# Kernel optimization log

Hardware: AMD Instinct MI355X
Metric: run time of the kernel (lower is better)

The kernel has to match this reference:

```python
import jax, jax.numpy as jnp
import numpy as np
import math

N = 20000          # real nodes (batch_size)
D = 256            # hidden_dim
H = 4              # num_heads
L = 3              # num_layers
E = 320000         # local edges
EXP_DEG = 4        # expander_degree
LN_EPS = 1e-5


def setup_inputs() -> dict:
    key = jax.random.key(0)
    ks = jax.random.split(key, 8)
    x = jax.random.normal(ks[0], (N, D), jnp.float32)
    rng = np.random.default_rng(0)
    edge_index = jnp.asarray(rng.integers(0, N, size=(2, E)), dtype=jnp.int32)
    # Expander: EXP_DEG//2 random permutations on N+1 nodes (incl. virtual node),
    # each contributing edges in both directions -> degree-EXP_DEG regular graph.
    n = N + 1
    perms = [rng.permutation(n) for _ in range(EXP_DEG // 2)]
    src = np.concatenate([np.arange(n) for _ in perms] + perms)
    dst = np.concatenate(perms + [np.arange(n) for _ in perms])
    exp_edge_index = jnp.asarray(np.stack([src, dst]), dtype=jnp.int32)
    s_in = 1.0 / math.sqrt(D)
    s_ffn = 1.0 / math.sqrt(4 * D)
    def w(k, shape, s):
        return jax.random.normal(k, shape, jnp.float32) * s
    params = {
        'Wqkv_loc': w(ks[1], (L, D, 3 * D), s_in), 'bqkv_loc': jnp.zeros((L, 3 * D), jnp.float32),
        'Wo_loc':   w(ks[2], (L, D, D), s_in),     'bo_loc':   jnp.zeros((L, D), jnp.float32),
        'Wqkv_exp': w(ks[3], (L, D, 3 * D), s_in), 'bqkv_exp': jnp.zeros((L, 3 * D), jnp.float32),
        'Wo_exp':   w(ks[4], (L, D, D), s_in),     'bo_exp':   jnp.zeros((L, D), jnp.float32),
        'ln_g': jnp.ones((L, D), jnp.float32),     'ln_b': jnp.zeros((L, D), jnp.float32),
        'W1': w(ks[5], (L, D, 4 * D), s_in),       'b1': jnp.zeros((L, 4 * D), jnp.float32),
        'W2': w(ks[6], (L, 4 * D, D), s_ffn),      'b2': jnp.zeros((L, D), jnp.float32),
    }
    return {'x': x, 'edge_index': edge_index, 'exp_edge_index': exp_edge_index, **params}


def _attention(h, src, dst, Wqkv, bqkv, Wo, bo):
    # Sparse multi-head attention over (src -> dst) edges with segment softmax per dst.
    n, d = h.shape
    dh = d // H
    qkv = (h @ Wqkv + bqkv).reshape(n, 3, H, dh)
    q, k, v = qkv[:, 0], qkv[:, 1], qkv[:, 2]            # [n, H, dh]
    score = (q[dst] * k[src]).sum(-1) / jnp.sqrt(jnp.float32(dh))  # [e, H]
    m = jax.ops.segment_max(score, dst, num_segments=n)  # [n, H]
    ex = jnp.exp(score - m[dst])
    denom = jax.ops.segment_sum(ex, dst, num_segments=n)
    alpha = ex / (denom[dst] + 1e-16)
    out = jax.ops.segment_sum(alpha[:, :, None] * v[src], dst, num_segments=n)  # [n, H, dh]
    return out.reshape(n, d) @ Wo + bo


def _layer_norm(x, g, b):
    mu = x.mean(-1, keepdims=True)
    var = ((x - mu) ** 2).mean(-1, keepdims=True)
    return (x - mu) * jax.lax.rsqrt(var + LN_EPS) * g + b


def reference(x, edge_index, exp_edge_index, Wqkv_loc, bqkv_loc, Wo_loc, bo_loc,
              Wqkv_exp, bqkv_exp, Wo_exp, bo_exp, ln_g, ln_b, W1, b1, W2, b2):
    n0 = x.shape[0]
    # VirtualNode transform: append one zero-feature node connected to/from all nodes.
    h = jnp.concatenate([x, jnp.zeros((1, x.shape[1]), x.dtype)], axis=0)
    ar = jnp.arange(n0, dtype=edge_index.dtype)
    vn = jnp.full((n0,), n0, dtype=edge_index.dtype)
    src = jnp.concatenate([edge_index[0], ar, vn])
    dst = jnp.concatenate([edge_index[1], vn, ar])
    esrc, edst = exp_edge_index[0], exp_edge_index[1]
    for l in range(L):  # fixed small number of structurally distinct layers
        res = h
        loc = _attention(h, src, dst, Wqkv_loc[l], bqkv_loc[l], Wo_loc[l], bo_loc[l])
        exp = _attention(h, esrc, edst, Wqkv_exp[l], bqkv_exp[l], Wo_exp[l], bo_exp[l])
        h = _layer_norm(res + loc + exp, ln_g[l], ln_b[l])
        h = h + (jax.nn.gelu(h @ W1[l] + b1[l], approximate=False) @ W2[l] + b2[l])
    return h[:n0]
```

## Files before the change

### kernel.cpp

```cpp
#include <hip/hip_runtime.h>
#include <stdint.h>

#define NREAL   20000
#define NNODES  20001
#define VN      20000
#define E_EDGES 320000
#define NEXP    80004
#define MPAD    20096
#define NVNW    320

typedef unsigned short u16;
typedef unsigned int   u32;
typedef __bf16 bf16x8 __attribute__((ext_vector_type(8)));
typedef float  f32x4  __attribute__((ext_vector_type(4)));
typedef u16    u16x8  __attribute__((ext_vector_type(8)));

__device__ __host__ __forceinline__ size_t fmoff(int row, int col, int LD) {
    return (size_t)(row >> 4) * ((size_t)LD * 16) + (size_t)((col >> 3) * 128)
         + (size_t)((row & 15) * 8) + (size_t)(col & 7);
}

__device__ __forceinline__ int qkv_perm(int n) {
    if (n < 256) return n;
    int u = n - 256;
    int part = u >> 8;
    int cl = u & 255;
    return 256 + (cl >> 2) * 8 + part * 4 + (cl & 3);
}

__device__ __forceinline__ float bf2f(u16 v) {
    union { u32 u; float f; } x; x.u = ((u32)v) << 16; return x.f;
}
__device__ __forceinline__ u16 f2bf(float f) {
    union { float f; u32 u; } x; x.f = f;
    u32 r = (x.u + 0x7fffu + ((x.u >> 16) & 1u)) >> 16;
    return (u16)r;
}
__device__ __forceinline__ float4 cvt4(ushort4 u) {
    return make_float4(bf2f(u.x), bf2f(u.y), bf2f(u.z), bf2f(u.w));
}
__device__ __forceinline__ float4 ld4bf(const u16* p) { return cvt4(*(const ushort4*)p); }
__device__ __forceinline__ float4 cvtk8(u16x8 r) {
    return make_float4(bf2f(r[0]), bf2f(r[1]), bf2f(r[2]), bf2f(r[3]));
}
__device__ __forceinline__ float4 cvtv8(u16x8 r) {
    return make_float4(bf2f(r[4]), bf2f(r[5]), bf2f(r[6]), bf2f(r[7]));
}


__global__ void hinit_kernel(const float* __restrict__ x, float* __restrict__ h,
                             u16* __restrict__ hb) {
    int idx = blockIdx.x * 256 + threadIdx.x;
    if (idx >= NNODES * 64) return;
    int row = idx >> 6, c0 = (idx & 63) * 4;
    float4 v = make_float4(0.f, 0.f, 0.f, 0.f);
    if (row < NREAL) v = *(const float4*)(x + (size_t)row * 256 + c0);
    *(float4*)(h + (size_t)row * 256 + c0) = v;
    ushort4 o;
    o.x = f2bf(v.x); o.y = f2bf(v.y); o.z = f2bf(v.z); o.w = f2bf(v.w);
    *(ushort4*)(hb + fmoff(row, c0, 256)) = o;
}

__global__ void init_kernel(int* cnt, int* fill, int* ecnt,
                            const float* __restrict__ bl, const float* __restrict__ be,
                            float* __restrict__ bcat,
                            const float* __restrict__ bol, const float* __restrict__ boe,
                            float* __restrict__ bsum) {
    int i = blockIdx.x * 256 + threadIdx.x;
    if (i < NREAL) { cnt[i] = 0; fill[i] = 0; }
    if (i < NNODES) ecnt[i] = 0;
    if (i < 3 * 1536) {
        int l = i / 1536, c = i - l * 1536;
        float v = (c < 768) ? bl[l * 768 + c] : be[l * 768 + c - 768];
        int cc = (c >= 768) ? c - 768 : c;
        int d = qkv_perm(cc) + ((c >= 768) ? 768 : 0);
        bcat[l * 1536 + d] = v;
    }
    if (i < 3 * 256) bsum[i] = bol[i] + boe[i];
}

__global__ void csr_count_kernel(const int* __restrict__ ei, int* __restrict__ cnt) {
    int e = blockIdx.x * 256 + threadIdx.x;
    if (e < E_EDGES) atomicAdd(&cnt[ei[E_EDGES + e]], 1);
}

__global__ void csr_scan_kernel(const int* __restrict__ cnt, int* __restrict__ indptr) {
    __shared__ int ssum[256];
    int t = threadIdx.x;
    int c0 = t * 79;
    int s = 0;
    for (int j = 0; j < 79; j++) {
        int i = c0 + j;
        if (i < NREAL) s += cnt[i];
    }
    ssum[t] = s;
    __syncthreads();
    for (int d2 = 1; d2 < 256; d2 <<= 1) {
        int v = (t >= d2) ? ssum[t - d2] : 0;
        __syncthreads();
        ssum[t] += v;
        __syncthreads();
    }
    int run = (t == 0) ? 0 : ssum[t - 1];
    for (int j = 0; j < 79; j++) {
        int i = c0 + j;
        if (i < NREAL) { indptr[i] = run; run += cnt[i]; }
    }
    if (t == 255) indptr[NREAL] = run;
}

__global__ void csr_scatter_kernel(const int* __restrict__ ei, const int* __restrict__ indptr,
                                   int* __restrict__ fill, int* __restrict__ srcs) {
    int e = blockIdx.x * 256 + threadIdx.x;
    if (e < E_EDGES) {
        int d = ei[E_EDGES + e];
        int pos = indptr[d] + atomicAdd(&fill[d], 1);
        srcs[pos] = ei[e];
    }
}

__global__ void exp_scatter_kernel(const int* __restrict__ eei, int* __restrict__ ecnt,
                                   int* __restrict__ esrcs) {
    int e = blockIdx.x * 256 + threadIdx.x;
    if (e < NEXP) {
        int d = eei[NEXP + e];
        int pos = atomicAdd(&ecnt[d], 1);
        esrcs[d * 4 + pos] = eei[e];
    }
}

__global__ void wconv_all_kernel(const float* __restrict__ WqkvL, const float* __restrict__ WqkvE,
                                 const float* __restrict__ WoL, const float* __restrict__ WoE,
                                 const float* __restrict__ W1, const float* __restrict__ W2,
                                 u16* __restrict__ out) {
    int i = blockIdx.x * 256 + threadIdx.x;
    if (i >= 3 * 1048576) return;
    int l = i / 1048576, r = i - l * 1048576;
    if (r >= 393216 && r < 524288) {
        int r2 = r - 393216;
        int k = r2 >> 8, n = r2 & 255;
        float v = (k < 256) ? WoL[(size_t)l * 65536 + k * 256 + n]
                            : WoE[(size_t)l * 65536 + (k - 256) * 256 + n];
        out[(size_t)l * 1048576 + 393216 + fmoff(n, k, 512)] = f2bf(v);
        return;
    }
    const float* src; int K, N; int base;
    if (r < 196608)      { src = WqkvL; K = 256;  N = 768;  base = 0; }
    else if (r < 393216) { src = WqkvE; K = 256;  N = 768;  base = 196608; }
    else if (r < 786432) { src = W1;    K = 256;  N = 1024; base = 524288; }
    else                 { src = W2;    K = 1024; N = 256;  base = 786432; }
    int r2 = r - base;
    int k = r2 / N, n = r2 - k * N;
    int d = (r < 393216) ? qkv_perm(n) : n;
    out[(size_t)l * 1048576 + base + fmoff(d, k, K)] = f2bf(src[(size_t)l * K * N + r2]);
}

__global__ __launch_bounds__(256) void qkv_rw(
    const u16* __restrict__ A, const u16* __restrict__ Bt, const float* __restrict__ bias,
    u16* __restrict__ Q0, u16* __restrict__ KV0,
    u16* __restrict__ Q1, u16* __restrict__ KV1, int M) {
    const int lin = blockIdx.x;
    const int mt = lin / 6, ns = lin - mt * 6;
    const int tm = mt * 64;
    if (tm >= M) return;
    const int tid = threadIdx.x;
    const int w = tid >> 6, lane = tid & 63;
    const int lm = lane & 15, q = lane >> 4;

    f32x4 acc[4][4];
#pragma unroll
    for (int a = 0; a < 4; a++)
#pragma unroll
        for (int b = 0; b < 4; b++) acc[a][b] = (f32x4)0.0f;

    const u16* apf[4];
    const u16* bpf[4];
#pragma unroll
    for (int mi = 0; mi < 4; mi++)
        apf[mi] = A + (size_t)(tm / 16 + mi) * 4096 + q * 128 + lm * 8;
#pragma unroll
    for (int ni = 0; ni < 4; ni++)
        bpf[ni] = Bt + (size_t)(ns * 16 + w * 4 + ni) * 4096 + q * 128 + lm * 8;

    bf16x8 sA[3][4], sB[3][4];
#pragma unroll
    for (int s = 0; s < 2; s++) {
#pragma unroll
        for (int mi = 0; mi < 4; mi++) sA[s][mi] = *(const bf16x8*)(apf[mi] + s * 512);
#pragma unroll
        for (int ni = 0; ni < 4; ni++) sB[s][ni] = *(const bf16x8*)(bpf[ni] + s * 512);
    }
#pragma unroll
    for (int i = 0; i < 8; i++) {
        const int cu = i % 3, pf = (i + 2) % 3;
        if (i + 2 < 8) {
#pragma unroll
            for (int mi = 0; mi < 4; mi++) sA[pf][mi] = *(const bf16x8*)(apf[mi] + (i + 2) * 512);
#pragma unroll
            for (int ni = 0; ni < 4; ni++) sB[pf][ni] = *(const bf16x8*)(bpf[ni] + (i + 2) * 512);
        }
#pragma unroll
        for (int mi = 0; mi < 4; mi++)
#pragma unroll
            for (int ni = 0; ni < 4; ni++)
                acc[mi][ni] = __builtin_amdgcn_mfma_f32_16x16x32_bf16(
                    sB[cu][ni], sA[cu][mi], acc[mi][ni], 0, 0, 0);
    }

    float4 b4[4];
#pragma unroll
    for (int ni = 0; ni < 4; ni++)
        b4[ni] = *(const float4*)(bias + ns * 256 + w * 64 + ni * 16 + q * 4);

#pragma unroll
    for (int mi = 0; mi < 4; mi++) {
        int grow = tm + mi * 16 + lm;
        if (grow >= M) continue;
#pragma unroll
        for (int ni = 0; ni < 4; ni++) {
            int gcol = ns * 256 + w * 64 + ni * 16 + q * 4;
            float v0 = acc[mi][ni][0] + b4[ni].x;
            float v1 = acc[mi][ni][1] + b4[ni].y;
            float v2 = acc[mi][ni][2] + b4[ni].z;
            float v3 = acc[mi][ni][3] + b4[ni].w;
            ushort4 o;
            o.x = f2bf(v0); o.y = f2bf(v1); o.z = f2bf(v2); o.w = f2bf(v3);
            u16* dst;
            if (gcol < 256)       dst = Q0  + (size_t)grow * 256 + gcol;
            else if (gcol < 768)  dst = KV0 + (size_t)grow * 512 + (gcol - 256);
            else if (gcol < 1024) dst = Q1  + (size_t)grow * 256 + (gcol - 768);
            else                  dst = KV1 + (size_t)grow * 512 + (gcol - 1024);
            *(ushort4*)dst = o;
        }
    }
}

__global__ __launch_bounds__(256) void ffn1_rw(
    const u16* __restrict__ A, const u16* __restrict__ Bt, const float* __restrict__ bias,
    u16* __restrict__ Cb, int M) {
    const int lin = blockIdx.x;
    const int mt = lin >> 2, ns = lin & 3;
    const int tm = mt * 64;
    if (tm >= M) return;
    const int tid = threadIdx.x;
    const int w = tid >> 6, lane = tid & 63;
    const int lm = lane & 15, q = lane >> 4;

    f32x4 acc[4][4];
#pragma unroll
    for (int a = 0; a < 4; a++)
#pragma unroll
        for (int b = 0; b < 4; b++) acc[a][b] = (f32x4)0.0f;

    const u16* apf[4];
    const u16* bpf[4];
#pragma unroll
    for (int mi = 0; mi < 4; mi++)
        apf[mi] = A + (size_t)(tm / 16 + mi) * 4096 + q * 128 + lm * 8;
#pragma unroll
    for (int ni = 0; ni < 4; ni++)
        bpf[ni] = Bt + (size_t)(ns * 16 + w * 4 + ni) * 4096 + q * 128 + lm * 8;

    bf16x8 sA[3][4], sB[3][4];
#pragma unroll
    for (int s = 0; s < 2; s++) {
#pragma unroll
        for (int mi = 0; mi < 4; mi++) sA[s][mi] = *(const bf16x8*)(apf[mi] + s * 512);
#pragma unroll
        for (int ni = 0; ni < 4; ni++) sB[s][ni] = *(const bf16x8*)(bpf[ni] + s * 512);
    }
#pragma unroll
    for (int i = 0; i < 8; i++) {
        const int cu = i % 3, pf = (i + 2) % 3;
        if (i + 2 < 8) {
#pragma unroll
            for (int mi = 0; mi < 4; mi++) sA[pf][mi] = *(const bf16x8*)(apf[mi] + (i + 2) * 512);
#pragma unroll
            for (int ni = 0; ni < 4; ni++) sB[pf][ni] = *(const bf16x8*)(bpf[ni] + (i + 2) * 512);
        }
#pragma unroll
        for (int mi = 0; mi < 4; mi++)
#pragma unroll
            for (int ni = 0; ni < 4; ni++)
                acc[mi][ni] = __builtin_amdgcn_mfma_f32_16x16x32_bf16(
                    sB[cu][ni], sA[cu][mi], acc[mi][ni], 0, 0, 0);
    }

    float4 b4[4];
#pragma unroll
    for (int ni = 0; ni < 4; ni++)
        b4[ni] = *(const float4*)(bias + ns * 256 + w * 64 + ni * 16 + q * 4);

#pragma unroll
    for (int mi = 0; mi < 4; mi++) {
        int grow = tm + mi * 16 + lm;
        if (grow >= M) continue;
#pragma unroll
        for (int ni = 0; ni < 4; ni++) {
            int gcol = ns * 256 + w * 64 + ni * 16 + q * 4;
            float v0 = acc[mi][ni][0] + b4[ni].x;
            float v1 = acc[mi][ni][1] + b4[ni].y;
            float v2 = acc[mi][ni][2] + b4[ni].z;
            float v3 = acc[mi][ni][3] + b4[ni].w;
            float g0, g1, g2, g3;
            {
                float u = 0.7978845608f * (v0 + 0.044715f * v0 * v0 * v0);
                g0 = 0.5f * v0 * (2.0f - 2.0f / (__expf(2.0f * u) + 1.0f));
            }
            {
                float u = 0.7978845608f * (v1 + 0.044715f * v1 * v1 * v1);
                g1 = 0.5f * v1 * (2.0f - 2.0f / (__expf(2.0f * u) + 1.0f));
            }
            {
                float u = 0.7978845608f * (v2 + 0.044715f * v2 * v2 * v2);
                g2 = 0.5f * v2 * (2.0f - 2.0f / (__expf(2.0f * u) + 1.0f));
            }
            {
                float u = 0.7978845608f * (v3 + 0.044715f * v3 * v3 * v3);
                g3 = 0.5f * v3 * (2.0f - 2.0f / (__expf(2.0f * u) + 1.0f));
            }
            ushort4 o;
            o.x = f2bf(g0); o.y = f2bf(g1); o.z = f2bf(g2); o.w = f2bf(g3);
            *(ushort4*)(Cb + fmoff(grow, gcol, 1024)) = o;
        }
    }
}

template <int EPI, int K, int MT>
__global__ __launch_bounds__(256) void gemm_fm(
    const u16* __restrict__ A, const u16* __restrict__ Bt, const float* __restrict__ bias,
    u16* Cb, float* Cf, const float* resid, int M, int Nout, int nby) {
    constexpr int MFR = MT / 32;
    constexpr int NK = K / 32;
    const int lin = blockIdx.x;
    const int xcd = lin & 7, sub = lin >> 3;
    const int mtile = xcd + 8 * (sub / nby);
    const int ntile = sub - (sub / nby) * nby;
    const int tm = mtile * MT, tn = ntile * 128;
    if (tm >= M) return;

    const int tid = threadIdx.x;
    const int w = tid >> 6, lane = tid & 63;
    const int lm = lane & 15, q = lane >> 4;
    const int mo = (w >> 1) * (MT / 2), no = (w & 1) * 64;

    f32x4 acc[MFR][4];
#pragma unroll
    for (int a = 0; a < MFR; a++)
#pragma unroll
        for (int b = 0; b < 4; b++) acc[a][b] = (f32x4)0.0f;

    const u16* apf[MFR];
    const u16* bpf[4];
#pragma unroll
    for (int t = 0; t < MFR; t++) {
        int p = (tm + mo) / 16 + t;
        apf[t] = A + (size_t)p * (16 * K) + q * 128 + lm * 8;
    }
#pragma unroll
    for (int n = 0; n < 4; n++) {
        int c = (tn + no) / 16 + n;
        bpf[n] = Bt + (size_t)c * (16 * K) + q * 128 + lm * 8;
    }

    bf16x8 sA[3][MFR], sB[3][4];
#pragma unroll
    for (int s = 0; s < 2 && s < NK; s++) {
#pragma unroll
        for (int t = 0; t < MFR; t++) sA[s][t] = *(const bf16x8*)(apf[t] + s * 512);
#pragma unroll
        for (int n = 0; n < 4; n++) sB[s][n] = *(const bf16x8*)(bpf[n] + s * 512);
    }
#pragma unroll
    for (int i = 0; i < NK; i++) {
        const int cu = i % 3, pf = (i + 2) % 3;
        if (i + 2 < NK) {
#pragma unroll
            for (int t = 0; t < MFR; t++) sA[pf][t] = *(const bf16x8*)(apf[t] + (i + 2) * 512);
#pragma unroll
            for (int n = 0; n < 4; n++) sB[pf][n] = *(const bf16x8*)(bpf[n] + (i + 2) * 512);
        }
#pragma unroll
        for (int mi = 0; mi < MFR; mi++)
#pragma unroll
            for (int ni = 0; ni < 4; ni++)
                acc[mi][ni] = __builtin_amdgcn_mfma_f32_16x16x32_bf16(
                    sB[cu][ni], sA[cu][mi], acc[mi][ni], 0, 0, 0);
    }

    float4 b4[4];
#pragma unroll
    for (int ni = 0; ni < 4; ni++)
        b4[ni] = *(const float4*)(bias + tn + no + ni * 16 + q * 4);

#pragma unroll
    for (int mi = 0; mi < MFR; mi++) {
        int grow = tm + mo + mi * 16 + lm;
        if constexpr (EPI == 4) { if (grow >= NREAL) continue; }
        else                    { if (grow >= M) continue; }
#pragma unroll
        for (int ni = 0; ni < 4; ni++) {
            int gcol = tn + no + ni * 16 + q * 4;
            float v0 = acc[mi][ni][0] + b4[ni].x;
            float v1 = acc[mi][ni][1] + b4[ni].y;
            float v2 = acc[mi][ni][2] + b4[ni].z;
            float v3 = acc[mi][ni][3] + b4[ni].w;
            size_t idx = (size_t)grow * Nout + gcol;
            if constexpr (EPI == 1) {
                *(float4*)(Cf + idx) = make_float4(v0, v1, v2, v3);
            } else if constexpr (EPI == 3) {
                float4 rv = *(const float4*)(resid + idx);
                float o0 = rv.x + v0, o1 = rv.y + v1, o2 = rv.z + v2, o3 = rv.w + v3;
                *(float4*)(Cf + idx) = make_float4(o0, o1, o2, o3);
                ushort4 o;
                o.x = f2bf(o0); o.y = f2bf(o1); o.z = f2bf(o2); o.w = f2bf(o3);
                *(ushort4*)(Cb + fmoff(grow, gcol, Nout)) = o;
            } else {
                float4 rv = *(const float4*)(resid + idx);
                *(float4*)(Cf + idx) = make_float4(rv.x + v0, rv.y + v1, rv.z + v2, rv.w + v3);
            }
        }
    }
}

__global__ void vn_merge_kernel(const float* __restrict__ part, u16* __restrict__ acat) {
    __shared__ float sm[4][64][6];
    int w = threadIdx.x >> 6, lane = threadIdx.x & 63;
    int h = lane >> 4;
    int off = (h << 6) + (lane & 15) * 4;
    float M = -1e30f, L = 0.0f;
    float ax = 0, ay = 0, az = 0, aw = 0;
    for (int p = w * 80; p < w * 80 + 80; p++) {
        const float* pp = part + (size_t)p * 264;
        float pm = pp[h], pl = pp[4 + h];
        float4 nm = *(const float4*)(pp + 8 + off);
        float Mn = fmaxf(M, pm);
        float s0 = __expf(M - Mn);
        float s1 = __expf(pm - Mn);
        ax = ax * s0 + nm.x * s1;
        ay = ay * s0 + nm.y * s1;
        az = az * s0 + nm.z * s1;
        aw = aw * s0 + nm.w * s1;
        L = L * s0 + pl * s1;
        M = Mn;
    }
    sm[w][lane][0] = M; sm[w][lane][1] = L;
    sm[w][lane][2] = ax; sm[w][lane][3] = ay;
    sm[w][lane][4] = az; sm[w][lane][5] = aw;
    __syncthreads();
    if (w == 0) {
        float M2 = -1e30f, L2 = 0.0f;
        float bx = 0, by = 0, bz = 0, bw = 0;
#pragma unroll
        for (int p = 0; p < 4; p++) {
            float pm = sm[p][lane][0], pl = sm[p][lane][1];
            float Mn = fmaxf(M2, pm);
            float s0 = __expf(M2 - Mn);
            float s1 = __expf(pm - Mn);
            bx = bx * s0 + sm[p][lane][2] * s1;
            by = by * s0 + sm[p][lane][3] * s1;
            bz = bz * s0 + sm[p][lane][4] * s1;
            bw = bw * s0 + sm[p][lane][5] * s1;
            L2 = L2 * s0 + pl * s1;
            M2 = Mn;
        }
        float inv = 1.0f / (L2 + 1e-16f);
        ushort4 o;
        o.x = f2bf(bx * inv); o.y = f2bf(by * inv);
        o.z = f2bf(bz * inv); o.w = f2bf(bw * inv);
        *(ushort4*)(acat + fmoff(VN, off, 512)) = o;
    }
}

__global__ void attn_fused_kernel(const u16* __restrict__ qb_loc, const u16* __restrict__ kv_loc,
                                  const u16* __restrict__ qb_exp, const u16* __restrict__ kv_exp,
                                  const int* __restrict__ indptr, const int* __restrict__ srcs,
                                  const int* __restrict__ esrcs,
                                  u16* __restrict__ acat, float* __restrict__ part) {
    int gw0 = (int)((blockIdx.x * (size_t)blockDim.x + threadIdx.x) >> 6);
    int gw = __builtin_amdgcn_readfirstlane(gw0);
    int lane = threadIdx.x & 63;
    int h = lane >> 4;
    int off = (h << 6) + (lane & 15) * 4;
    int coff = (off >> 2) * 8;

    if (gw < NVNW) {
        int wv = gw;
        float4 qv = ld4bf(qb_loc + (size_t)VN * 256 + off);
        float m = -1e30f, l = 0.0f;
        float ax = 0, ay = 0, az = 0, aw = 0;
        for (int i = wv; i < NREAL; i += NVNW) {
            u16x8 r = *(const u16x8*)(kv_loc + (size_t)i * 512 + coff);
            float4 k4 = cvtk8(r);
            float4 v4 = cvtv8(r);
            float s = qv.x * k4.x + qv.y * k4.y + qv.z * k4.z + qv.w * k4.w;
            s += __shfl_xor(s, 1); s += __shfl_xor(s, 2);
            s += __shfl_xor(s, 4); s += __shfl_xor(s, 8);
            float sc = s * 0.125f;
            float mn = fmaxf(m, sc);
            float fold = __expf(m - mn);
            float ee = __expf(sc - mn);
            ax = ax * fold + v4.x * ee;
            ay = ay * fold + v4.y * ee;
            az = az * fold + v4.z * ee;
            aw = aw * fold + v4.w * ee;
            l = l * fold + ee;
            m = mn;
        }
        float* pp = part + (size_t)wv * 264;
        if ((lane & 15) == 0) { pp[h] = m; pp[4 + h] = l; }
        *(float4*)(pp + 8 + off) = make_float4(ax, ay, az, aw);
        return;
    }
    gw -= NVNW;

    const u16 *qb, *kv;
    const int* sl;
    int node, beg, deg, tot, cbase;
    if (gw < NREAL) {
        node = gw; qb = qb_loc; kv = kv_loc; sl = srcs; cbase = 0;
        beg = indptr[node]; deg = indptr[node + 1] - beg; tot = deg + 1;
    } else if (gw < NREAL + NNODES) {
        node = gw - NREAL;
        qb = qb_exp; kv = kv_exp; sl = esrcs; cbase = 256;
        beg = node * 4; deg = 4; tot = 4;
    } else {
        return;
    }

    float4 qv = ld4bf(qb + (size_t)node * 256 + off);
    float m = -1e30f, l = 0.0f;
    float ax = 0, ay = 0, az = 0, aw = 0;

    if (tot <= 4) {
        u16x8 raw[4];
#pragma unroll
        for (int j = 0; j < 4; j++) {
            int s = (j < deg) ? sl[beg + j] : VN;
            raw[j] = *(const u16x8*)(kv + (size_t)s * 512 + coff);
        }
        float sc[4];
#pragma unroll
        for (int j = 0; j < 4; j++) {
            float4 k4 = cvtk8(raw[j]);
            float p = qv.x * k4.x + qv.y * k4.y + qv.z * k4.z + qv.w * k4.w;
            p += __shfl_xor(p, 1); p += __shfl_xor(p, 2);
            p += __shfl_xor(p, 4); p += __shfl_xor(p, 8);
            sc[j] = (j < tot) ? p * 0.125f : -1e30f;
        }
        float mn = fmaxf(fmaxf(sc[0], sc[1]), fmaxf(sc[2], sc[3]));
#pragma unroll
        for (int j = 0; j < 4; j++) {
            float ee = __expf(sc[j] - mn);
            float4 v4 = cvtv8(raw[j]);
            ax += v4.x * ee; ay += v4.y * ee; az += v4.z * ee; aw += v4.w * ee;
            l += ee;
        }
        m = mn;
    } else {
        const int nch = (tot + 7) >> 3;
        u16x8 rA[8], rB[8];
#pragma unroll
        for (int j = 0; j < 8; j++) {
            int s = (j < deg) ? sl[beg + j] : VN;
            rA[j] = *(const u16x8*)(kv + (size_t)s * 512 + coff);
        }
        for (int c = 0; c < nch; c++) {
            if (c + 1 < nch) {
                const int e0n = (c + 1) * 8;
#pragma unroll
                for (int j = 0; j < 8; j++) {
                    int e = e0n + j;
                    int s = (e < deg) ? sl[beg + e] : VN;
                    rB[j] = *(const u16x8*)(kv + (size_t)s * 512 + coff);
                }
            }
            const int e0 = c * 8;
            float sc[8];
#pragma unroll
            for (int j = 0; j < 8; j++) {
                float4 k4 = cvtk8(rA[j]);
                float p = qv.x * k4.x + qv.y * k4.y + qv.z * k4.z + qv.w * k4.w;
                p += __shfl_xor(p, 1); p += __shfl_xor(p, 2);
                p += __shfl_xor(p, 4); p += __shfl_xor(p, 8);
                sc[j] = (e0 + j < tot) ? p * 0.125f : -1e30f;
            }
            float cmax = fmaxf(fmaxf(fmaxf(sc[0], sc[1]), fmaxf(sc[2], sc[3])),
                               fmaxf(fmaxf(sc[4], sc[5]), fmaxf(sc[6], sc[7])));
            float mn = fmaxf(m, cmax);
            float fold = __expf(m - mn);
            ax *= fold; ay *= fold; az *= fold; aw *= fold; l *= fold;
#pragma unroll
            for (int j = 0; j < 8; j++) {
                float ee = __expf(sc[j] - mn);
                float4 v4 = cvtv8(rA[j]);
                ax += v4.x * ee; ay += v4.y * ee; az += v4.z * ee; aw += v4.w * ee;
                l += ee;
            }
            m = mn;
#pragma unroll
            for (int j = 0; j < 8; j++) rA[j] = rB[j];
        }
    }
    float inv = 1.0f / (l + 1e-16f);
    ushort4 o;
    o.x = f2bf(ax * inv); o.y = f2bf(ay * inv);
    o.z = f2bf(az * inv); o.w = f2bf(aw * inv);
    *(ushort4*)(acat + fmoff(node, cbase + off, 512)) = o;
}

__global__ void ln_kernel(const float* hin, const float* __restrict__ asum,
                          const float* __restrict__ g, const float* __restrict__ b,
                          float* hout, u16* __restrict__ hb) {
    int row = blockIdx.x * 4 + (threadIdx.x >> 6);
    if (row >= NNODES) return;
    int lane = threadIdx.x & 63;
    size_t base = (size_t)row * 256 + lane * 4;
    float4 xv = *(const float4*)(hin + base);
    float4 av = *(const float4*)(asum + base);
    xv.x += av.x; xv.y += av.y; xv.z += av.z; xv.w += av.w;
    float s = xv.x + xv.y + xv.z + xv.w;
#pragma unroll
    for (int o = 1; o < 64; o <<= 1) s += __shfl_xor(s, o);
    float mu = s * (1.0f / 256.0f);
    float dx = xv.x - mu, dy = xv.y - mu, dz = xv.z - mu, dw = xv.w - mu;
    float ss = dx * dx + dy * dy + dz * dz + dw * dw;
#pragma unroll
    for (int o = 1; o < 64; o <<= 1) ss += __shfl_xor(ss, o);
    float var = ss * (1.0f / 256.0f);
    float inv = 1.0f / sqrtf(var + 1e-5f);
    float4 gv = *(const float4*)(g + lane * 4);
    float4 bv = *(const float4*)(b + lane * 4);
    float4 y;
    y.x = dx * inv * gv.x + bv.x;
    y.y = dy * inv * gv.y + bv.y;
    y.z = dz * inv * gv.z + bv.z;
    y.w = dw * inv * gv.w + bv.w;
    *(float4*)(hout + base) = y;
    ushort4 o4;
    o4.x = f2bf(y.x); o4.y = f2bf(y.y); o4.z = f2bf(y.z); o4.w = f2bf(y.w);
    *(ushort4*)(hb + fmoff(row, lane * 4, 256)) = o4;
}


extern "C" void kernel_launch(void* const* d_in, const int* in_sizes, int n_in,
                              void* d_out, int out_size, void* d_ws, size_t ws_size,
                              hipStream_t stream) {
    (void)in_sizes; (void)n_in; (void)out_size;
    const float* x        = (const float*)d_in[0];
    const int*   ei       = (const int*)d_in[1];
    const int*   eei      = (const int*)d_in[2];
    const float* Wqkv_loc = (const float*)d_in[3];
    const float* bqkv_loc = (const float*)d_in[4];
    const float* Wo_loc   = (const float*)d_in[5];
    const float* bo_loc   = (const float*)d_in[6];
    const float* Wqkv_exp = (const float*)d_in[7];
    const float* bqkv_exp = (const float*)d_in[8];
    const float* Wo_exp   = (const float*)d_in[9];
    const float* bo_exp   = (const float*)d_in[10];
    const float* ln_g     = (const float*)d_in[11];
    const float* ln_b     = (const float*)d_in[12];
    const float* W1       = (const float*)d_in[13];
    const float* b1       = (const float*)d_in[14];
    const float* W2       = (const float*)d_in[15];
    const float* b2       = (const float*)d_in[16];

    char* wsp = (char*)d_ws;
    size_t off = 0;
    auto carve = [&](size_t bytes) -> void* {
        void* p = wsp + off;
        off += (bytes + 255) & ~(size_t)255;
        return p;
    };
    float* h_f    = (float*)carve((size_t)NNODES * 256 * 4);
    u16*   h_b    = (u16*)carve((size_t)MPAD * 256 * 2);
    u16*   qb_loc = (u16*)carve((size_t)NNODES * 256 * 2);
    u16*   kv_loc = (u16*)carve((size_t)NNODES * 512 * 2);
    u16*   qb_exp = (u16*)carve((size_t)NNODES * 256 * 2);
    u16*   kv_exp = (u16*)carve((size_t)NNODES * 512 * 2);
    u16*   acat   = (u16*)carve((size_t)MPAD * 512 * 2);
    float* asum   = (float*)carve((size_t)NNODES * 256 * 4);
    u16*   wbf    = (u16*)carve((size_t)3 * 1048576 * 2);
    float* bcat   = (float*)carve((size_t)3 * 1536 * 4);
    float* bsum   = (float*)carve((size_t)3 * 256 * 4);
    int*   cnt    = (int*)carve((size_t)NREAL * 4);
    int*   indptr = (int*)carve((size_t)(NREAL + 1) * 4);
    int*   fill   = (int*)carve((size_t)NREAL * 4);
    int*   srcs   = (int*)carve((size_t)E_EDGES * 4);
    int*   ecnt   = (int*)carve((size_t)NNODES * 4);
    int*   esrcs  = (int*)carve((size_t)NNODES * 4 * 4);
    float* part   = (float*)carve((size_t)NVNW * 264 * 4);
    u16*   mid_d  = (u16*)carve((size_t)MPAD * 1024 * 2);
    u16*   mid    = (ws_size >= off) ? mid_d : qb_loc;

    hinit_kernel<<<(NNODES * 64 + 255) / 256, 256, 0, stream>>>(x, h_f, h_b);
    init_kernel<<<(NNODES + 255) / 256, 256, 0, stream>>>(
        cnt, fill, ecnt, bqkv_loc, bqkv_exp, bcat, bo_loc, bo_exp, bsum);
    csr_count_kernel<<<(E_EDGES + 255) / 256, 256, 0, stream>>>(ei, cnt);
    csr_scan_kernel<<<1, 256, 0, stream>>>(cnt, indptr);
    csr_scatter_kernel<<<(E_EDGES + 255) / 256, 256, 0, stream>>>(ei, indptr, fill, srcs);
    exp_scatter_kernel<<<(NEXP + 255) / 256, 256, 0, stream>>>(eei, ecnt, esrcs);
    wconv_all_kernel<<<(3 * 1048576 + 255) / 256, 256, 0, stream>>>(
        Wqkv_loc, Wqkv_exp, Wo_loc, Wo_exp, W1, W2, wbf);

    const int NBM64 = 320;
    const int ATTN_BLOCKS = (NVNW + NREAL + NNODES + 3) / 4;
    const int QKV_BLOCKS = (MPAD / 64) * 6;

    for (int l = 0; l < 3; l++) {
        const u16* wqkvC = wbf + (size_t)l * 1048576 + 0;
        const u16* wocat = wbf + (size_t)l * 1048576 + 393216;
        const u16* w1T   = wbf + (size_t)l * 1048576 + 524288;
        const u16* w2T   = wbf + (size_t)l * 1048576 + 786432;

        qkv_rw<<<QKV_BLOCKS, 256, 0, stream>>>(
            h_b, wqkvC, bcat + l * 1536,
            qb_loc, kv_loc, qb_exp, kv_exp, NNODES);

        attn_fused_kernel<<<ATTN_BLOCKS, 256, 0, stream>>>(
            qb_loc, kv_loc, qb_exp, kv_exp, indptr, srcs, esrcs, acat, part);
        vn_merge_kernel<<<1, 256, 0, stream>>>(part, acat);

        gemm_fm<1, 512, 64><<<NBM64 * 2, 256, 0, stream>>>(
            acat, wocat, bsum + l * 256, nullptr, asum, nullptr, NNODES, 256, 2);

        ln_kernel<<<(NNODES + 3) / 4, 256, 0, stream>>>(
            h_f, asum, ln_g + l * 256, ln_b + l * 256, h_f, h_b);

        ffn1_rw<<<320 * 4, 256, 0, stream>>>(
            h_b, w1T, b1 + l * 1024, mid, NNODES);

        if (l < 2) {
            gemm_fm<3, 1024, 64><<<NBM64 * 2, 256, 0, stream>>>(
                mid, w2T, b2 + l * 256, h_b, h_f, h_f, NNODES, 256, 2);
        } else {
            gemm_fm<4, 1024, 64><<<NBM64 * 2, 256, 0, stream>>>(
                mid, w2T, b2 + l * 256, nullptr, (float*)d_out, h_f, NNODES, 256, 2);
        }
    }
}
```

Baseline: 822.8 us.

## Fuse output projection with LayerNorm and use full-row 32-row GEMM tiles

Replaces the Wo GEMM plus separate LayerNorm kernel with one kernel that computes a 32x256 full-row tile, adds the residual, and does the row LayerNorm in-register via cross-wave shared-memory reductions. This removes the fp32 asum intermediate and one launch per layer. The W2 GEMM is also retiled to full 256-column rows with 32-row blocks. Each block now reads all of the weight matrix, and the grid has fewer, larger blocks with a different XCD mapping.

```diff
diff --git a/kernel.cpp b/kernel.cpp
--- a/kernel.cpp
+++ b/kernel.cpp
@@ -326,62 +326,53 @@
     }
 }
 
-template <int EPI, int K, int MT>
-__global__ __launch_bounds__(256) void gemm_fm(
+__global__ __launch_bounds__(256) void wo_ln_rw(
     const u16* __restrict__ A, const u16* __restrict__ Bt, const float* __restrict__ bias,
-    u16* Cb, float* Cf, const float* resid, int M, int Nout, int nby) {
-    constexpr int MFR = MT / 32;
-    constexpr int NK = K / 32;
-    const int lin = blockIdx.x;
-    const int xcd = lin & 7, sub = lin >> 3;
-    const int mtile = xcd + 8 * (sub / nby);
-    const int ntile = sub - (sub / nby) * nby;
-    const int tm = mtile * MT, tn = ntile * 128;
+    const float* __restrict__ resid, const float* __restrict__ g,
+    const float* __restrict__ bvec, float* __restrict__ hout, u16* __restrict__ hb,
+    int M) {
+    __shared__ float smS[32][4];
+    __shared__ float smQ[32][4];
+    const int tm = blockIdx.x * 32;
     if (tm >= M) return;
-
     const int tid = threadIdx.x;
     const int w = tid >> 6, lane = tid & 63;
     const int lm = lane & 15, q = lane >> 4;
-    const int mo = (w >> 1) * (MT / 2), no = (w & 1) * 64;
-
-    f32x4 acc[MFR][4];
-#pragma unroll
-    for (int a = 0; a < MFR; a++)
+
+    f32x4 acc[2][4];
+#pragma unroll
+    for (int a = 0; a < 2; a++)
 #pragma unroll
         for (int b = 0; b < 4; b++) acc[a][b] = (f32x4)0.0f;
 
-    const u16* apf[MFR];
+    const u16* apf[2];
     const u16* bpf[4];
 #pragma unroll
-    for (int t = 0; t < MFR; t++) {
-        int p = (tm + mo) / 16 + t;
-        apf[t] = A + (size_t)p * (16 * K) + q * 128 + lm * 8;
-    }
-#pragma unroll
-    for (int n = 0; n < 4; n++) {
-        int c = (tn + no) / 16 + n;
-        bpf[n] = Bt + (size_t)c * (16 * K) + q * 128 + lm * 8;
-    }
-
-    bf16x8 sA[3][MFR], sB[3][4];
-#pragma unroll
-    for (int s = 0; s < 2 && s < NK; s++) {
-#pragma unroll
-        for (int t = 0; t < MFR; t++) sA[s][t] = *(const bf16x8*)(apf[t] + s * 512);
-#pragma unroll
-        for (int n = 0; n < 4; n++) sB[s][n] = *(const bf16x8*)(bpf[n] + s * 512);
-    }
-#pragma unroll
-    for (int i = 0; i < NK; i++) {
+    for (int mi = 0; mi < 2; mi++)
+        apf[mi] = A + (size_t)(tm / 16 + mi) * 8192 + q * 128 + lm * 8;
+#pragma unroll
+    for (int ni = 0; ni < 4; ni++)
+        bpf[ni] = Bt + (size_t)(w * 4 + ni) * 8192 + q * 128 + lm * 8;
+
+    bf16x8 sA[3][2], sB[3][4];
+#pragma unroll
+    for (int s = 0; s < 2; s++) {
+#pragma unroll
+        for (int mi = 0; mi < 2; mi++) sA[s][mi] = *(const bf16x8*)(apf[mi] + s * 512);
+#pragma unroll
+        for (int ni = 0; ni < 4; ni++) sB[s][ni] = *(const bf16x8*)(bpf[ni] + s * 512);
+    }
+#pragma unroll
+    for (int i = 0; i < 16; i++) {
         const int cu = i % 3, pf = (i + 2) % 3;
-        if (i + 2 < NK) {
-#pragma unroll
-            for (int t = 0; t < MFR; t++) sA[pf][t] = *(const bf16x8*)(apf[t] + (i + 2) * 512);
-#pragma unroll
-            for (int n = 0; n < 4; n++) sB[pf][n] = *(const bf16x8*)(bpf[n] + (i + 2) * 512);
-        }
-#pragma unroll
-        for (int mi = 0; mi < MFR; mi++)
+        if (i + 2 < 16) {
+#pragma unroll
+            for (int mi = 0; mi < 2; mi++) sA[pf][mi] = *(const bf16x8*)(apf[mi] + (i + 2) * 512);
+#pragma unroll
+            for (int ni = 0; ni < 4; ni++) sB[pf][ni] = *(const bf16x8*)(bpf[ni] + (i + 2) * 512);
+        }
+#pragma unroll
+        for (int mi = 0; mi < 2; mi++)
 #pragma unroll
             for (int ni = 0; ni < 4; ni++)
                 acc[mi][ni] = __builtin_amdgcn_mfma_f32_16x16x32_bf16(
@@ -391,33 +382,166 @@
     float4 b4[4];
 #pragma unroll
     for (int ni = 0; ni < 4; ni++)
-        b4[ni] = *(const float4*)(bias + tn + no + ni * 16 + q * 4);
-
-#pragma unroll
-    for (int mi = 0; mi < MFR; mi++) {
-        int grow = tm + mo + mi * 16 + lm;
-        if constexpr (EPI == 4) { if (grow >= NREAL) continue; }
-        else                    { if (grow >= M) continue; }
+        b4[ni] = *(const float4*)(bias + w * 64 + ni * 16 + q * 4);
+#pragma unroll
+    for (int mi = 0; mi < 2; mi++) {
+        int grow = tm + mi * 16 + lm;
 #pragma unroll
         for (int ni = 0; ni < 4; ni++) {
-            int gcol = tn + no + ni * 16 + q * 4;
+            int gcol = w * 64 + ni * 16 + q * 4;
+            size_t idx = (size_t)grow * 256 + gcol;
+            float4 rv = *(const float4*)(resid + idx);
+            acc[mi][ni][0] = rv.x + (acc[mi][ni][0] + b4[ni].x);
+            acc[mi][ni][1] = rv.y + (acc[mi][ni][1] + b4[ni].y);
+            acc[mi][ni][2] = rv.z + (acc[mi][ni][2] + b4[ni].z);
+            acc[mi][ni][3] = rv.w + (acc[mi][ni][3] + b4[ni].w);
+        }
+    }
+
+    float s1[2];
+#pragma unroll
+    for (int mi = 0; mi < 2; mi++) {
+        float s = 0.f;
+#pragma unroll
+        for (int ni = 0; ni < 4; ni++)
+            s += acc[mi][ni][0] + acc[mi][ni][1] + acc[mi][ni][2] + acc[mi][ni][3];
+        s += __shfl_xor(s, 16); s += __shfl_xor(s, 32);
+        s1[mi] = s;
+    }
+    if (lane < 16) {
+        smS[lm][w] = s1[0];
+        smS[16 + lm][w] = s1[1];
+    }
+    __syncthreads();
+    float mu[2];
+#pragma unroll
+    for (int mi = 0; mi < 2; mi++) {
+        int r = mi * 16 + lm;
+        mu[mi] = (smS[r][0] + smS[r][1] + smS[r][2] + smS[r][3]) * (1.0f / 256.0f);
+    }
+    float s2[2];
+#pragma unroll
+    for (int mi = 0; mi < 2; mi++) {
+        float s = 0.f;
+#pragma unroll
+        for (int ni = 0; ni < 4; ni++) {
+            float d0 = acc[mi][ni][0] - mu[mi];
+            float d1 = acc[mi][ni][1] - mu[mi];
+            float d2 = acc[mi][ni][2] - mu[mi];
+            float d3 = acc[mi][ni][3] - mu[mi];
+            s += d0 * d0 + d1 * d1 + d2 * d2 + d3 * d3;
+        }
+        s += __shfl_xor(s, 16); s += __shfl_xor(s, 32);
+        s2[mi] = s;
+    }
+    if (lane < 16) {
+        smQ[lm][w] = s2[0];
+        smQ[16 + lm][w] = s2[1];
+    }
+    __syncthreads();
+    float rinv[2];
+#pragma unroll
+    for (int mi = 0; mi < 2; mi++) {
+        int r = mi * 16 + lm;
+        float var = (smQ[r][0] + smQ[r][1] + smQ[r][2] + smQ[r][3]) * (1.0f / 256.0f);
+        rinv[mi] = 1.0f / sqrtf(var + 1e-5f);
+    }
+#pragma unroll
+    for (int mi = 0; mi < 2; mi++) {
+        int grow = tm + mi * 16 + lm;
+        if (grow >= M) continue;
+#pragma unroll
+        for (int ni = 0; ni < 4; ni++) {
+            int gcol = w * 64 + ni * 16 + q * 4;
+            float4 gv = *(const float4*)(g + gcol);
+            float4 bv = *(const float4*)(bvec + gcol);
+            float4 y;
+            y.x = (acc[mi][ni][0] - mu[mi]) * rinv[mi] * gv.x + bv.x;
+            y.y = (acc[mi][ni][1] - mu[mi]) * rinv[mi] * gv.y + bv.y;
+            y.z = (acc[mi][ni][2] - mu[mi]) * rinv[mi] * gv.z + bv.z;
+            y.w = (acc[mi][ni][3] - mu[mi]) * rinv[mi] * gv.w + bv.w;
+            *(float4*)(hout + (size_t)grow * 256 + gcol) = y;
+            ushort4 o;
+            o.x = f2bf(y.x); o.y = f2bf(y.y); o.z = f2bf(y.z); o.w = f2bf(y.w);
+            *(ushort4*)(hb + fmoff(grow, gcol, 256)) = o;
+        }
+    }
+}
+
+__global__ __launch_bounds__(256) void w2_rw(
+    const u16* __restrict__ A, const u16* __restrict__ Bt, const float* __restrict__ bias,
+    const float* __restrict__ resid, float* __restrict__ Cf, u16* __restrict__ Cb,
+    int last, int M) {
+    const int tm = blockIdx.x * 32;
+    if (tm >= M) return;
+    const int tid = threadIdx.x;
+    const int w = tid >> 6, lane = tid & 63;
+    const int lm = lane & 15, q = lane >> 4;
+
+    f32x4 acc[2][4];
+#pragma unroll
+    for (int a = 0; a < 2; a++)
+#pragma unroll
+        for (int b = 0; b < 4; b++) acc[a][b] = (f32x4)0.0f;
+
+    const u16* apf[2];
+    const u16* bpf[4];
+#pragma unroll
+    for (int mi = 0; mi < 2; mi++)
+        apf[mi] = A + (size_t)(tm / 16 + mi) * 16384 + q * 128 + lm * 8;
+#pragma unroll
+    for (int ni = 0; ni < 4; ni++)
+        bpf[ni] = Bt + (size_t)(w * 4 + ni) * 16384 + q * 128 + lm * 8;
+
+    bf16x8 sA[3][2], sB[3][4];
+#pragma unroll
+    for (int s = 0; s < 2; s++) {
+#pragma unroll
+        for (int mi = 0; mi < 2; mi++) sA[s][mi] = *(const bf16x8*)(apf[mi] + s * 512);
+#pragma unroll
+        for (int ni = 0; ni < 4; ni++) sB[s][ni] = *(const bf16x8*)(bpf[ni] + s * 512);
+    }
+#pragma unroll
+    for (int i = 0; i < 32; i++) {
+        const int cu = i % 3, pf = (i + 2) % 3;
+        if (i + 2 < 32) {
+#pragma unroll
+            for (int mi = 0; mi < 2; mi++) sA[pf][mi] = *(const bf16x8*)(apf[mi] + (i + 2) * 512);
+#pragma unroll
+            for (int ni = 0; ni < 4; ni++) sB[pf][ni] = *(const bf16x8*)(bpf[ni] + (i + 2) * 512);
+        }
+#pragma unroll
+        for (int mi = 0; mi < 2; mi++)
+#pragma unroll
+            for (int ni = 0; ni < 4; ni++)
+                acc[mi][ni] = __builtin_amdgcn_mfma_f32_16x16x32_bf16(
+                    sB[cu][ni], sA[cu][mi], acc[mi][ni], 0, 0, 0);
+    }
+
+    float4 b4[4];
+#pragma unroll
+    for (int ni = 0; ni < 4; ni++)
+        b4[ni] = *(const float4*)(bias + w * 64 + ni * 16 + q * 4);
+
+#pragma unroll
+    for (int mi = 0; mi < 2; mi++) {
+        int grow = tm + mi * 16 + lm;
+        if (grow >= (last ? NREAL : M)) continue;
+#pragma unroll
+        for (int ni = 0; ni < 4; ni++) {
+            int gcol = w * 64 + ni * 16 + q * 4;
             float v0 = acc[mi][ni][0] + b4[ni].x;
             float v1 = acc[mi][ni][1] + b4[ni].y;
             float v2 = acc[mi][ni][2] + b4[ni].z;
             float v3 = acc[mi][ni][3] + b4[ni].w;
-            size_t idx = (size_t)grow * Nout + gcol;
-            if constexpr (EPI == 1) {
-                *(float4*)(Cf + idx) = make_float4(v0, v1, v2, v3);
-            } else if constexpr (EPI == 3) {
-                float4 rv = *(const float4*)(resid + idx);
-                float o0 = rv.x + v0, o1 = rv.y + v1, o2 = rv.z + v2, o3 = rv.w + v3;
-                *(float4*)(Cf + idx) = make_float4(o0, o1, o2, o3);
+            size_t idx = (size_t)grow * 256 + gcol;
+            float4 rv = *(const float4*)(resid + idx);
+            float o0 = rv.x + v0, o1 = rv.y + v1, o2 = rv.z + v2, o3 = rv.w + v3;
+            *(float4*)(Cf + idx) = make_float4(o0, o1, o2, o3);
+            if (!last) {
                 ushort4 o;
                 o.x = f2bf(o0); o.y = f2bf(o1); o.z = f2bf(o2); o.w = f2bf(o3);
-                *(ushort4*)(Cb + fmoff(grow, gcol, Nout)) = o;
-            } else {
-                float4 rv = *(const float4*)(resid + idx);
-                *(float4*)(Cf + idx) = make_float4(rv.x + v0, rv.y + v1, rv.z + v2, rv.w + v3);
+                *(ushort4*)(Cb + fmoff(grow, gcol, 256)) = o;
             }
         }
     }
@@ -609,39 +733,6 @@
     *(ushort4*)(acat + fmoff(node, cbase + off, 512)) = o;
 }
 
-__global__ void ln_kernel(const float* hin, const float* __restrict__ asum,
-                          const float* __restrict__ g, const float* __restrict__ b,
-                          float* hout, u16* __restrict__ hb) {
-    int row = blockIdx.x * 4 + (threadIdx.x >> 6);
-    if (row >= NNODES) return;
-    int lane = threadIdx.x & 63;
-    size_t base = (size_t)row * 256 + lane * 4;
-    float4 xv = *(const float4*)(hin + base);
-    float4 av = *(const float4*)(asum + base);
-    xv.x += av.x; xv.y += av.y; xv.z += av.z; xv.w += av.w;
-    float s = xv.x + xv.y + xv.z + xv.w;
-#pragma unroll
-    for (int o = 1; o < 64; o <<= 1) s += __shfl_xor(s, o);
-    float mu = s * (1.0f / 256.0f);
-    float dx = xv.x - mu, dy = xv.y - mu, dz = xv.z - mu, dw = xv.w - mu;
-    float ss = dx * dx + dy * dy + dz * dz + dw * dw;
-#pragma unroll
-    for (int o = 1; o < 64; o <<= 1) ss += __shfl_xor(ss, o);
-    float var = ss * (1.0f / 256.0f);
-    float inv = 1.0f / sqrtf(var + 1e-5f);
-    float4 gv = *(const float4*)(g + lane * 4);
-    float4 bv = *(const float4*)(b + lane * 4);
-    float4 y;
-    y.x = dx * inv * gv.x + bv.x;
-    y.y = dy * inv * gv.y + bv.y;
-    y.z = dz * inv * gv.z + bv.z;
-    y.w = dw * inv * gv.w + bv.w;
-    *(float4*)(hout + base) = y;
-    ushort4 o4;
-    o4.x = f2bf(y.x); o4.y = f2bf(y.y); o4.z = f2bf(y.z); o4.w = f2bf(y.w);
-    *(ushort4*)(hb + fmoff(row, lane * 4, 256)) = o4;
-}
-
 
 extern "C" void kernel_launch(void* const* d_in, const int* in_sizes, int n_in,
                               void* d_out, int out_size, void* d_ws, size_t ws_size,
@@ -679,7 +770,6 @@
     u16*   qb_exp = (u16*)carve((size_t)NNODES * 256 * 2);
     u16*   kv_exp = (u16*)carve((size_t)NNODES * 512 * 2);
     u16*   acat   = (u16*)carve((size_t)MPAD * 512 * 2);
-    float* asum   = (float*)carve((size_t)NNODES * 256 * 4);
     u16*   wbf    = (u16*)carve((size_t)3 * 1048576 * 2);
     float* bcat   = (float*)carve((size_t)3 * 1536 * 4);
     float* bsum   = (float*)carve((size_t)3 * 256 * 4);
@@ -703,9 +793,9 @@
     wconv_all_kernel<<<(3 * 1048576 + 255) / 256, 256, 0, stream>>>(
         Wqkv_loc, Wqkv_exp, Wo_loc, Wo_exp, W1, W2, wbf);
 
-    const int NBM64 = 320;
     const int ATTN_BLOCKS = (NVNW + NREAL + NNODES + 3) / 4;
     const int QKV_BLOCKS = (MPAD / 64) * 6;
+    const int RW32_BLOCKS = MPAD / 32;
 
     for (int l = 0; l < 3; l++) {
         const u16* wqkvC = wbf + (size_t)l * 1048576 + 0;
@@ -721,21 +811,19 @@
             qb_loc, kv_loc, qb_exp, kv_exp, indptr, srcs, esrcs, acat, part);
         vn_merge_kernel<<<1, 256, 0, stream>>>(part, acat);
 
-        gemm_fm<1, 512, 64><<<NBM64 * 2, 256, 0, stream>>>(
-            acat, wocat, bsum + l * 256, nullptr, asum, nullptr, NNODES, 256, 2);
-
-        ln_kernel<<<(NNODES + 3) / 4, 256, 0, stream>>>(
-            h_f, asum, ln_g + l * 256, ln_b + l * 256, h_f, h_b);
+        wo_ln_rw<<<RW32_BLOCKS, 256, 0, stream>>>(
+            acat, wocat, bsum + l * 256, h_f,
+            ln_g + l * 256, ln_b + l * 256, h_f, h_b, NNODES);
 
         ffn1_rw<<<320 * 4, 256, 0, stream>>>(
             h_b, w1T, b1 + l * 1024, mid, NNODES);
 
         if (l < 2) {
-            gemm_fm<3, 1024, 64><<<NBM64 * 2, 256, 0, stream>>>(
-                mid, w2T, b2 + l * 256, h_b, h_f, h_f, NNODES, 256, 2);
+            w2_rw<<<RW32_BLOCKS, 256, 0, stream>>>(
+                mid, w2T, b2 + l * 256, h_f, h_f, h_b, 0, NNODES);
         } else {
-            gemm_fm<4, 1024, 64><<<NBM64 * 2, 256, 0, stream>>>(
-                mid, w2T, b2 + l * 256, nullptr, (float*)d_out, h_f, NNODES, 256, 2);
-        }
-    }
-}
+            w2_rw<<<RW32_BLOCKS, 256, 0, stream>>>(
+                mid, w2T, b2 + l * 256, h_f, (float*)d_out, nullptr, 1, NNODES);
+        }
+    }
+}
```

After: 793.7 us. 3.5% less time.
